# Optimization experiments

Hardware: AMD Instinct MI355X
Metric: run time of the kernel (lower is better)

The kernel has to match this reference:

```python
import jax, jax.numpy as jnp
import numpy as np


def decode_e4m3(bits):
    """Decode raw FP8 E4M3 byte patterns (int32 in [0,256)) to float32.

    Layout: 1 sign bit, 4 exponent bits (bias 7), 3 mantissa bits.
    exp==0 -> subnormal: mant/8 * 2^-6. The NaN pattern (exp==15, man==7)
    is remapped to the max normal magnitude 448 to keep the reference
    NaN-free for randomized inputs.
    """
    b = bits.astype(jnp.int32)
    sign = jnp.where((b & 0x80) != 0, -1.0, 1.0).astype(jnp.float32)
    exp = (b >> 3) & 0xF
    man = (b & 0x7).astype(jnp.float32)
    # remap NaN encoding (exp=15, man=7) to max normal 448 = (1+6/8)*2^8
    man = jnp.where((exp == 15) & (man == 7.0), 6.0, man)
    sub = man * jnp.float32(2.0 ** -9)                     # man/8 * 2^-6
    norm = (1.0 + man / 8.0) * jnp.exp2((exp - 7).astype(jnp.float32))
    return sign * jnp.where(exp == 0, sub, norm)


def setup_inputs() -> dict:
    key = jax.random.key(0)
    k1, k2, k3, k4 = jax.random.split(key, 4)
    T, D_IN, D_OUT = 8192, 4096, 8192  # tokens (2x4096), in_features, out_features
    x = jax.random.normal(k1, (T, D_IN), dtype=jnp.float32)
    weight_fp8 = jax.random.randint(k2, (D_OUT, D_IN), 0, 256, dtype=jnp.int32)
    weight_scales = jax.random.uniform(k3, (D_OUT,), dtype=jnp.float32)
    bias = jax.random.normal(k4, (D_OUT,), dtype=jnp.float32)
    return {"x": x, "weight_fp8": weight_fp8, "weight_scales": weight_scales, "bias": bias}


def reference(x, weight_fp8, weight_scales, bias):
    # Fused FP8 dequant + GEMM + bias: W = decode(w_fp8) * scale[:, None]
    w = decode_e4m3(weight_fp8) * weight_scales[:, None]   # [out, in]
    return jnp.einsum("ti,oi->to", x, w) + bias[None, :]
```

## Files before the change

### kernel.cpp

```cpp
#include <hip/hip_runtime.h>

using short8 = __attribute__((ext_vector_type(8))) short;
using bf16x8 = __attribute__((ext_vector_type(8))) __bf16;
using f32x4  = __attribute__((ext_vector_type(4))) float;

__device__ __forceinline__ void gload_lds16(const void* g, void* l) {
  __builtin_amdgcn_global_load_lds(
      (const __attribute__((address_space(1))) void*)g,
      (__attribute__((address_space(3))) void*)l, 16, 0, 0);
}


__device__ __forceinline__ float dec_e4m3(int b) {
  int e = (b >> 3) & 15;
  int m = b & 7;
  if (e == 15 && m == 7) m = 6;
  float v;
  if (e) v = (1.0f + (float)m * 0.125f) * __uint_as_float((unsigned)(e + 120) << 23);
  else   v = (float)m * 0.001953125f;
  return (b & 0x80) ? -v : v;
}

__global__ void dec_w_kernel(const int* __restrict__ wq,
                             unsigned short* __restrict__ wb, int n8) {
  int i = blockIdx.x * blockDim.x + threadIdx.x;
  if (i >= n8) return;
  const int4* p = (const int4*)wq + (size_t)i * 2;
  int4 a = p[0], b4 = p[1];
  int bv[8] = {a.x, a.y, a.z, a.w, b4.x, b4.y, b4.z, b4.w};
  short8 r;
#pragma unroll
  for (int j = 0; j < 8; ++j) {
    float f = dec_e4m3(bv[j]);
    r[j] = (short)(__float_as_uint(f) >> 16);
  }
  *(short8*)(wb + (size_t)i * 8) = r;
}

__global__ void cvt_x_kernel(const float* __restrict__ x,
                             unsigned short* __restrict__ xb, int n8) {
  int i = blockIdx.x * blockDim.x + threadIdx.x;
  if (i >= n8) return;
  const float4* p = (const float4*)x + (size_t)i * 2;
  float4 a = p[0], b4 = p[1];
  float v[8] = {a.x, a.y, a.z, a.w, b4.x, b4.y, b4.z, b4.w};
  short8 r;
#pragma unroll
  for (int j = 0; j < 8; ++j) {
    unsigned u = __float_as_uint(v[j]);
    u += 0x7FFFu + ((u >> 16) & 1u);
    r[j] = (short)(u >> 16);
  }
  *(short8*)(xb + (size_t)i * 8) = r;
}


#define NOPV ((void)0)
#define VM6 asm volatile("s_waitcnt vmcnt(6)" ::: "memory")
#define VM0 asm volatile("s_waitcnt vmcnt(0)" ::: "memory")

#define STAGE_A(LBUF, KT, J) do { \
    const char* _g = gAb + (size_t)(KT) * 128u; \
    gload_lds16(_g + (size_t)((J) * 64) * Kb, (LBUF) + ((J) * 64) * 128 + tdA); \
    gload_lds16(_g + (size_t)(128 + (J) * 64) * Kb, (LBUF) + (128 + (J) * 64) * 128 + tdA); \
  } while (0)

#define STAGE_B(LBUF, KT, J) do { \
    const char* _g = gBb + (size_t)(KT) * 128u; \
    gload_lds16(_g + (size_t)((J) * 32) * Kb, (LBUF) + ((J) * 32) * 128 + tdB); \
    gload_lds16(_g + (size_t)(128 + (J) * 32) * Kb, (LBUF) + (128 + (J) * 32) * 128 + tdB); \
  } while (0)

#define PHASE(QM, QN, DOA, DOB, STAGE, LGK8, VM) { \
    if (DOA) { \
      _Pragma("unroll") \
      for (int mi = 0; mi < 4; ++mi) { \
        const char* _b = lA + (size_t)(arow + (QM) * 64 + mi * 16) * 128; \
        a[mi][0] = *(const bf16x8*)(_b + fo0); \
        a[mi][1] = *(const bf16x8*)(_b + fo1); \
      } \
    } \
    if (DOB) { \
      _Pragma("unroll") \
      for (int ni = 0; ni < 2; ++ni) { \
        const char* _b = lB + (size_t)(brow + ((QN) * 2 + ni) * 16) * 128; \
        b[(QN) * 2 + ni][0] = *(const bf16x8*)(_b + fo0); \
        b[(QN) * 2 + ni][1] = *(const bf16x8*)(_b + fo1); \
      } \
    } \
    STAGE; \
    if (LGK8) asm volatile("s_waitcnt lgkmcnt(8)" ::: "memory"); \
    __builtin_amdgcn_s_barrier(); \
    asm volatile("s_waitcnt lgkmcnt(0)" ::: "memory"); \
    __builtin_amdgcn_sched_barrier(0); \
    __builtin_amdgcn_s_setprio(1); \
    _Pragma("unroll") \
    for (int mi = 0; mi < 4; ++mi) \
      _Pragma("unroll") \
      for (int ni = 0; ni < 2; ++ni) \
        _Pragma("unroll") \
        for (int ks = 0; ks < 2; ++ks) \
          acc[(QM) * 4 + mi][(QN) * 2 + ni] = __builtin_amdgcn_mfma_f32_16x16x32_bf16( \
              a[mi][ks], b[(QN) * 2 + ni][ks], acc[(QM) * 4 + mi][(QN) * 2 + ni], 0, 0, 0); \
    __builtin_amdgcn_s_setprio(0); \
    VM; \
    __builtin_amdgcn_s_barrier(); \
  }

__global__ __launch_bounds__(512, 2) void gemm256_kernel(
    const unsigned short* __restrict__ A, const unsigned short* __restrict__ B,
    const float* __restrict__ scale, const float* __restrict__ bias,
    float* __restrict__ out, int T, int K, int N) {
  extern __shared__ char lds[];
  char* const lA0 = lds;
  char* const lB0 = lds + 32768;
  char* const lA1 = lds + 65536;
  char* const lB1 = lds + 98304;

  const int nbn = N >> 8;
  const int nbm = T >> 8;
  const int nwg = nbm * nbn;
  int bm, bn;
  if ((nbn & 31) == 0 && (nwg & 7) == 0) {
    const int xcd = blockIdx.x & 7, off = blockIdx.x >> 3;
    const int bpc = nbm << 2;
    const int col = xcd * (nbn >> 5) + off / bpc;
    const int c   = off % bpc;
    bm = (c >> 2) << 8;
    bn = (col * 4 + (c & 3)) << 8;
  } else {
    const int q = nwg >> 3, r = nwg & 7;
    const int xcd = blockIdx.x & 7, off = blockIdx.x >> 3;
    const int swz = (xcd < r ? xcd * (q + 1) : r * (q + 1) + (xcd - r) * q) + off;
    bm = (swz / nbn) << 8;
    bn = (swz % nbn) << 8;
  }

  const int tid = threadIdx.x;
  const int wave = tid >> 6, lane = tid & 63;
  const int wm = wave >> 2, wn = wave & 3;
  const int nt = K >> 6;
  const size_t Kb = (size_t)K * 2;

  const int trow = tid >> 3;
  const int gcol = ((tid & 7) * 16) ^ (((tid >> 3) & 7) << 4);
  const int bmap = ((tid & 256) ? 64 : 0) + ((tid >> 6) & 3) * 8 + ((tid >> 3) & 7);
  const char* gAb = (const char*)A + (size_t)(bm + trow) * Kb + gcol;
  const char* gBb = (const char*)B + (size_t)(bn + bmap) * Kb + gcol;
  const int tdA = tid * 16;
  const int tdB = bmap * 128 + (tid & 7) * 16;

  const int g16 = lane >> 4, l8 = lane & 7;
  const int fo0 = ((g16 ^ l8) << 4);
  const int fo1 = fo0 ^ 64;
  const int arow = wm * 128 + (lane & 15);
  const int brow = wn * 64 + (lane & 15);

  f32x4 acc[8][4] = {};
  bf16x8 a[4][2], b[4][2];
  const char *lA, *lB;

  STAGE_A(lA0, 0, 0);
  STAGE_B(lB0, 0, 0);
  STAGE_B(lB0, 0, 1);
  STAGE_A(lA0, 0, 1);
  STAGE_A(lA1, 1, 0);
  STAGE_B(lB1, 1, 0);
  STAGE_B(lB1, 1, 1);
  VM6;
  __builtin_amdgcn_s_barrier();

  int t = 0;
  for (; t + 3 < nt; t += 2) {
    lA = lA0; lB = lB0;
    PHASE(0, 0, 1, 1, STAGE_A(lA1, t + 1, 1), 1, NOPV)
    PHASE(0, 1, 0, 1, STAGE_A(lA0, t + 2, 0), 0, NOPV)
    PHASE(1, 1, 1, 0, STAGE_B(lB0, t + 2, 0), 0, NOPV)
    PHASE(1, 0, 0, 0, STAGE_B(lB0, t + 2, 1), 0, VM6)
    lA = lA1; lB = lB1;
    PHASE(0, 0, 1, 1, STAGE_A(lA0, t + 2, 1), 1, NOPV)
    PHASE(0, 1, 0, 1, STAGE_A(lA1, t + 3, 0), 0, NOPV)
    PHASE(1, 1, 1, 0, STAGE_B(lB1, t + 3, 0), 0, NOPV)
    PHASE(1, 0, 0, 0, STAGE_B(lB1, t + 3, 1), 0, VM6)
  }
  lA = lA0; lB = lB0;
  PHASE(0, 0, 1, 1, STAGE_A(lA1, t + 1, 1), 1, NOPV)
  PHASE(0, 1, 0, 1, NOPV, 0, NOPV)
  PHASE(1, 1, 1, 0, NOPV, 0, NOPV)
  PHASE(1, 0, 0, 0, NOPV, 0, VM0)
  lA = lA1; lB = lB1;
  PHASE(0, 0, 1, 1, NOPV, 1, NOPV)
  PHASE(0, 1, 0, 1, NOPV, 0, NOPV)
  PHASE(1, 1, 1, 0, NOPV, 0, NOPV)
  PHASE(1, 0, 0, 0, NOPV, 0, NOPV)

  const int ccol = bn + wn * 64 + (lane & 15);
  const int crow = bm + wm * 128 + ((lane >> 4) << 2);
#pragma unroll
  for (int ni = 0; ni < 4; ++ni) {
    const int o = ccol + ni * 16;
    const float sc = scale[o], bi = bias[o];
#pragma unroll
    for (int mi = 0; mi < 8; ++mi) {
#pragma unroll
      for (int rr = 0; rr < 4; ++rr) {
        __builtin_nontemporal_store(acc[mi][ni][rr] * sc + bi,
                                    &out[(size_t)(crow + mi * 16 + rr) * N + o]);
      }
    }
  }
}


#define BM 128
#define BN 128
#define BK 64

__global__ __launch_bounds__(256) void gemm_bf16_kernel(
    const unsigned short* __restrict__ A, const unsigned short* __restrict__ B,
    const float* __restrict__ scale, const float* __restrict__ bias,
    float* __restrict__ out, int T, int K, int N) {
  __shared__ __align__(16) unsigned short lsA[BM * BK];
  __shared__ __align__(16) unsigned short lsB[BN * BK];

  const int nbn = N / BN;
  const int nwg = (T / BM) * nbn;
  const int q = nwg >> 3, r = nwg & 7;
  const int xcd = blockIdx.x & 7, off = blockIdx.x >> 3;
  const int swz = (xcd < r ? xcd * (q + 1) : r * (q + 1) + (xcd - r) * q) + off;
  const int bm = (swz / nbn) * BM;
  const int bn = (swz % nbn) * BN;

  const int tid = threadIdx.x;
  const int wave = tid >> 6, lane = tid & 63;
  const int wm = (wave >> 1) * 64, wn = (wave & 1) * 64;

  f32x4 acc[4][4] = {};

  const int srow = (wave << 3) + (lane >> 3);
  const int scolb = (lane & 7) * 16;
  const size_t Kb = (size_t)K * 2;
  const char* gA = (const char*)A + (size_t)bm * Kb + scolb;
  const char* gB = (const char*)B + (size_t)bn * Kb + scolb;
  char* laddrA = (char*)lsA + wave * 1024;
  char* laddrB = (char*)lsB + wave * 1024;

  for (int k0 = 0; k0 < K; k0 += BK) {
    const char* pa = gA + (size_t)k0 * 2;
    const char* pb = gB + (size_t)k0 * 2;
#pragma unroll
    for (int s = 0; s < 4; ++s) {
      int row = s * 32 + srow;
      gload_lds16(pa + (size_t)row * Kb, laddrA + s * 4096);
      gload_lds16(pb + (size_t)row * Kb, laddrB + s * 4096);
    }
    __syncthreads();

    const int arow2 = wm + (lane & 15);
    const int brow2 = wn + (lane & 15);
#pragma unroll
    for (int kk = 0; kk < BK; kk += 32) {
      const int kcol = kk + ((lane >> 4) << 3);
      bf16x8 af[4], bfr[4];
#pragma unroll
      for (int i = 0; i < 4; ++i)
        af[i] = *(const bf16x8*)(lsA + (size_t)(arow2 + i * 16) * BK + kcol);
#pragma unroll
      for (int i = 0; i < 4; ++i)
        bfr[i] = *(const bf16x8*)(lsB + (size_t)(brow2 + i * 16) * BK + kcol);
#pragma unroll
      for (int mi = 0; mi < 4; ++mi)
#pragma unroll
        for (int ni = 0; ni < 4; ++ni)
          acc[mi][ni] = __builtin_amdgcn_mfma_f32_16x16x32_bf16(
              af[mi], bfr[ni], acc[mi][ni], 0, 0, 0);
    }
    __syncthreads();
  }

  const int ccol = bn + wn + (lane & 15);
  const int crow0 = bm + wm + ((lane >> 4) << 2);
#pragma unroll
  for (int ni = 0; ni < 4; ++ni) {
    const int o = ccol + ni * 16;
    const float sc = scale[o], bi = bias[o];
#pragma unroll
    for (int mi = 0; mi < 4; ++mi) {
#pragma unroll
      for (int rr = 0; rr < 4; ++rr) {
        const int t2 = crow0 + mi * 16 + rr;
        out[(size_t)t2 * N + o] = acc[mi][ni][rr] * sc + bi;
      }
    }
  }
}


__global__ void naive_kernel(const float* __restrict__ X, const int* __restrict__ Wq,
                             const float* __restrict__ sc, const float* __restrict__ bs,
                             float* __restrict__ out, int T, int K, int N) {
  __shared__ float xt[16][16];
  __shared__ float wt[16][17];
  const int tx = threadIdx.x & 15, ty = threadIdx.x >> 4;
  const int t = blockIdx.y * 16 + ty, o = blockIdx.x * 16 + tx;
  float acc = 0.f;
  for (int k0 = 0; k0 < K; k0 += 16) {
    xt[ty][tx] = X[(size_t)t * K + k0 + tx];
    wt[ty][tx] = dec_e4m3(Wq[(size_t)(blockIdx.x * 16 + ty) * K + k0 + tx]);
    __syncthreads();
#pragma unroll
    for (int kk = 0; kk < 16; ++kk) acc += xt[ty][kk] * wt[tx][kk];
    __syncthreads();
  }
  out[(size_t)t * N + o] = acc * sc[o] + bs[o];
}

extern "C" void kernel_launch(void* const* d_in, const int* in_sizes, int n_in,
                              void* d_out, int out_size, void* d_ws, size_t ws_size,
                              hipStream_t stream) {
  const float* x  = (const float*)d_in[0];
  const int*   wq = (const int*)d_in[1];
  const float* sc = (const float*)d_in[2];
  const float* bi = (const float*)d_in[3];
  float* out = (float*)d_out;

  const int DOUT = in_sizes[2];
  const int DIN  = in_sizes[1] / DOUT;
  const int T    = in_sizes[0] / DIN;

  const size_t need = ((size_t)T * DIN + (size_t)DOUT * DIN) * 2;
  const bool ok256 = (T % 256 == 0) && (DOUT % 256 == 0) && (DIN % 256 == 0);
  const bool ok128 = (T % BM == 0) && (DOUT % BN == 0) && (DIN % BK == 0);

  if (ws_size >= need && (ok256 || ok128)) {
    unsigned short* xb = (unsigned short*)d_ws;
    unsigned short* wb = xb + (size_t)T * DIN;
    const int nx8 = (int)((size_t)T * DIN / 8);
    const int nw8 = (int)((size_t)DOUT * DIN / 8);
    cvt_x_kernel<<<(nx8 + 255) / 256, 256, 0, stream>>>(x, xb, nx8);
    dec_w_kernel<<<(nw8 + 255) / 256, 256, 0, stream>>>(wq, wb, nw8);
    if (ok256) {
      dim3 grid((T >> 8) * (DOUT >> 8));
      gemm256_kernel<<<grid, 512, 131072, stream>>>(xb, wb, sc, bi, out, T, DIN, DOUT);
    } else {
      dim3 grid((T / BM) * (DOUT / BN));
      gemm_bf16_kernel<<<grid, 256, 0, stream>>>(xb, wb, sc, bi, out, T, DIN, DOUT);
    }
  } else {
    dim3 g(DOUT / 16, T / 16);
    naive_kernel<<<g, 256, 0, stream>>>(x, wq, sc, bi, out, T, DIN, DOUT);
  }
}
```

Before: 517.3 us.

## Chain four M-tiles per workgroup and prefetch next tile during tail

The 256x256 GEMM grid shrinks by a factor of four. Each workgroup now walks four consecutive M tiles for a fixed N column. The loads for the next tile's first K stage are issued inside the last compute phases of the current tile, so the prologue and epilogue overlap with MMA work. Scale and bias are loaded once up front, and the XCD mapping is rewritten so each XCD owns a set of N columns. The aim is to cut per-block launch, prologue and epilogue bubbles and to reuse the B tile. The cost is fewer, longer workgroups, which makes load balance and tail effects more sensitive.

```diff
diff --git a/kernel.cpp b/kernel.cpp
--- a/kernel.cpp
+++ b/kernel.cpp
@@ -59,14 +59,14 @@
 #define VM6 asm volatile("s_waitcnt vmcnt(6)" ::: "memory")
 #define VM0 asm volatile("s_waitcnt vmcnt(0)" ::: "memory")
 
-#define STAGE_A(LBUF, KT, J) do { \
-    const char* _g = gAb + (size_t)(KT) * 128u; \
+#define STAGE_A(GP, LBUF, KT, J) do { \
+    const char* _g = (GP) + (size_t)(KT) * 128u; \
     gload_lds16(_g + (size_t)((J) * 64) * Kb, (LBUF) + ((J) * 64) * 128 + tdA); \
     gload_lds16(_g + (size_t)(128 + (J) * 64) * Kb, (LBUF) + (128 + (J) * 64) * 128 + tdA); \
   } while (0)
 
-#define STAGE_B(LBUF, KT, J) do { \
-    const char* _g = gBb + (size_t)(KT) * 128u; \
+#define STAGE_B(GP, LBUF, KT, J) do { \
+    const char* _g = (GP) + (size_t)(KT) * 128u; \
     gload_lds16(_g + (size_t)((J) * 32) * Kb, (LBUF) + ((J) * 32) * 128 + tdB); \
     gload_lds16(_g + (size_t)(128 + (J) * 32) * Kb, (LBUF) + (128 + (J) * 32) * 128 + tdB); \
   } while (0)
@@ -119,21 +119,24 @@
 
   const int nbn = N >> 8;
   const int nbm = T >> 8;
-  const int nwg = nbm * nbn;
-  int bm, bn;
-  if ((nbn & 31) == 0 && (nwg & 7) == 0) {
+  int bm, bn, CH;
+  if (((nbm & 3) == 0) && ((nbn & 7) == 0) &&
+      (int)gridDim.x == (nbm >> 2) * nbn) {
     const int xcd = blockIdx.x & 7, off = blockIdx.x >> 3;
-    const int bpc = nbm << 2;
-    const int col = xcd * (nbn >> 5) + off / bpc;
-    const int c   = off % bpc;
-    bm = (c >> 2) << 8;
-    bn = (col * 4 + (c & 3)) << 8;
+    const int cpx = nbn >> 3;
+    const int col = xcd * cpx + (off % cpx);
+    const int ci  = off / cpx;
+    bm = (ci * 4) << 8;
+    bn = col << 8;
+    CH = 4;
   } else {
+    const int nwg = nbm * nbn;
     const int q = nwg >> 3, r = nwg & 7;
     const int xcd = blockIdx.x & 7, off = blockIdx.x >> 3;
     const int swz = (xcd < r ? xcd * (q + 1) : r * (q + 1) + (xcd - r) * q) + off;
     bm = (swz / nbn) << 8;
     bn = (swz % nbn) << 8;
+    CH = 1;
   }
 
   const int tid = threadIdx.x;
@@ -156,57 +159,85 @@
   const int arow = wm * 128 + (lane & 15);
   const int brow = wn * 64 + (lane & 15);
 
+  const int ccol = bn + wn * 64 + (lane & 15);
+  int crow = bm + wm * 128 + ((lane >> 4) << 2);
+  float scv[4], biv[4];
+#pragma unroll
+  for (int ni = 0; ni < 4; ++ni) {
+    scv[ni] = scale[ccol + ni * 16];
+    biv[ni] = bias[ccol + ni * 16];
+  }
+
   f32x4 acc[8][4] = {};
   bf16x8 a[4][2], b[4][2];
   const char *lA, *lB;
 
-  STAGE_A(lA0, 0, 0);
-  STAGE_B(lB0, 0, 0);
-  STAGE_B(lB0, 0, 1);
-  STAGE_A(lA0, 0, 1);
-  STAGE_A(lA1, 1, 0);
-  STAGE_B(lB1, 1, 0);
-  STAGE_B(lB1, 1, 1);
-  VM6;
-  __builtin_amdgcn_s_barrier();
-
-  int t = 0;
-  for (; t + 3 < nt; t += 2) {
+  for (int ch = 0; ch < CH; ++ch) {
+    const bool more = (ch + 1 < CH);
+    const char* gAn = gAb + (size_t)256 * Kb;
+
+    if (ch == 0) {
+      STAGE_A(gAb, lA0, 0, 0);
+      STAGE_B(gBb, lB0, 0, 0);
+      STAGE_B(gBb, lB0, 0, 1);
+      STAGE_A(gAb, lA0, 0, 1);
+      STAGE_A(gAb, lA1, 1, 0);
+      STAGE_B(gBb, lB1, 1, 0);
+      STAGE_B(gBb, lB1, 1, 1);
+      VM6;
+      __builtin_amdgcn_s_barrier();
+    }
+
+    int t = 0;
+    for (; t + 3 < nt; t += 2) {
+      lA = lA0; lB = lB0;
+      PHASE(0, 0, 1, 1, STAGE_A(gAb, lA1, t + 1, 1), 1, NOPV)
+      PHASE(0, 1, 0, 1, STAGE_A(gAb, lA0, t + 2, 0), 0, NOPV)
+      PHASE(1, 1, 1, 0, STAGE_B(gBb, lB0, t + 2, 0), 0, NOPV)
+      PHASE(1, 0, 0, 0, STAGE_B(gBb, lB0, t + 2, 1), 0, VM6)
+      lA = lA1; lB = lB1;
+      PHASE(0, 0, 1, 1, STAGE_A(gAb, lA0, t + 2, 1), 1, NOPV)
+      PHASE(0, 1, 0, 1, STAGE_A(gAb, lA1, t + 3, 0), 0, NOPV)
+      PHASE(1, 1, 1, 0, STAGE_B(gBb, lB1, t + 3, 0), 0, NOPV)
+      PHASE(1, 0, 0, 0, STAGE_B(gBb, lB1, t + 3, 1), 0, VM6)
+    }
     lA = lA0; lB = lB0;
-    PHASE(0, 0, 1, 1, STAGE_A(lA1, t + 1, 1), 1, NOPV)
-    PHASE(0, 1, 0, 1, STAGE_A(lA0, t + 2, 0), 0, NOPV)
-    PHASE(1, 1, 1, 0, STAGE_B(lB0, t + 2, 0), 0, NOPV)
-    PHASE(1, 0, 0, 0, STAGE_B(lB0, t + 2, 1), 0, VM6)
+    PHASE(0, 0, 1, 1, STAGE_A(gAb, lA1, t + 1, 1), 1, NOPV)
+    PHASE(0, 1, 0, 1, NOPV, 0, NOPV)
+    PHASE(1, 1, 1, 0, NOPV, 0, NOPV)
+    PHASE(1, 0, 0, 0, NOPV, 0, VM0)
     lA = lA1; lB = lB1;
-    PHASE(0, 0, 1, 1, STAGE_A(lA0, t + 2, 1), 1, NOPV)
-    PHASE(0, 1, 0, 1, STAGE_A(lA1, t + 3, 0), 0, NOPV)
-    PHASE(1, 1, 1, 0, STAGE_B(lB1, t + 3, 0), 0, NOPV)
-    PHASE(1, 0, 0, 0, STAGE_B(lB1, t + 3, 1), 0, VM6)
-  }
-  lA = lA0; lB = lB0;
-  PHASE(0, 0, 1, 1, STAGE_A(lA1, t + 1, 1), 1, NOPV)
-  PHASE(0, 1, 0, 1, NOPV, 0, NOPV)
-  PHASE(1, 1, 1, 0, NOPV, 0, NOPV)
-  PHASE(1, 0, 0, 0, NOPV, 0, VM0)
-  lA = lA1; lB = lB1;
-  PHASE(0, 0, 1, 1, NOPV, 1, NOPV)
-  PHASE(0, 1, 0, 1, NOPV, 0, NOPV)
-  PHASE(1, 1, 1, 0, NOPV, 0, NOPV)
-  PHASE(1, 0, 0, 0, NOPV, 0, NOPV)
-
-  const int ccol = bn + wn * 64 + (lane & 15);
-  const int crow = bm + wm * 128 + ((lane >> 4) << 2);
-#pragma unroll
-  for (int ni = 0; ni < 4; ++ni) {
-    const int o = ccol + ni * 16;
-    const float sc = scale[o], bi = bias[o];
-#pragma unroll
-    for (int mi = 0; mi < 8; ++mi) {
-#pragma unroll
-      for (int rr = 0; rr < 4; ++rr) {
-        __builtin_nontemporal_store(acc[mi][ni][rr] * sc + bi,
-                                    &out[(size_t)(crow + mi * 16 + rr) * N + o]);
+    PHASE(0, 0, 1, 1, { if (more) STAGE_A(gAn, lA0, 0, 0); }, 1, NOPV)
+    PHASE(0, 1, 0, 1, { if (more) STAGE_B(gBb, lB0, 0, 0); }, 0, NOPV)
+    PHASE(1, 1, 1, 0, { if (more) STAGE_B(gBb, lB0, 0, 1); }, 0, NOPV)
+    PHASE(1, 0, 0, 0, { if (more) STAGE_A(gAn, lA0, 0, 1); }, 0, NOPV)
+
+#pragma unroll
+    for (int ni = 0; ni < 4; ++ni) {
+      const int o = ccol + ni * 16;
+#pragma unroll
+      for (int mi = 0; mi < 8; ++mi) {
+#pragma unroll
+        for (int rr = 0; rr < 4; ++rr) {
+          __builtin_nontemporal_store(acc[mi][ni][rr] * scv[ni] + biv[ni],
+                                      &out[(size_t)(crow + mi * 16 + rr) * N + o]);
+        }
       }
+    }
+
+    if (more) {
+#pragma unroll
+      for (int mi = 0; mi < 8; ++mi)
+#pragma unroll
+        for (int ni = 0; ni < 4; ++ni)
+          acc[mi][ni] = (f32x4){0.f, 0.f, 0.f, 0.f};
+      STAGE_A(gAn, lA1, 1, 0);
+      STAGE_B(gBb, lB1, 1, 0);
+      STAGE_B(gBb, lB1, 1, 1);
+      VM6;
+      __builtin_amdgcn_s_barrier();
+      gAb = gAn;
+      crow += 256;
     }
   }
 }
@@ -340,7 +371,9 @@
     cvt_x_kernel<<<(nx8 + 255) / 256, 256, 0, stream>>>(x, xb, nx8);
     dec_w_kernel<<<(nw8 + 255) / 256, 256, 0, stream>>>(wq, wb, nw8);
     if (ok256) {
-      dim3 grid((T >> 8) * (DOUT >> 8));
+      const int nbm = T >> 8, nbn = DOUT >> 8;
+      const bool okchain = ((nbm & 3) == 0) && ((nbn & 7) == 0);
+      const int grid = okchain ? (nbm >> 2) * nbn : nbm * nbn;
       gemm256_kernel<<<grid, 512, 131072, stream>>>(xb, wb, sc, bi, out, T, DIN, DOUT);
     } else {
       dim3 grid((T / BM) * (DOUT / BN));
```

After: 515.2 us. No clear change (-0.4%).
